# Kernel optimization log

Hardware: AMD Instinct MI355X
Metric: run time of the kernel (lower is better)

## Reference

```python
import math
import jax, jax.numpy as jnp
import numpy as np

B, T, E, H, D = 2, 2048, 1024, 16, 64


def setup_inputs() -> dict:
    key = jax.random.key(0)
    ks = jax.random.split(key, 6)
    x = jax.random.normal(ks[0], (B, T, E), dtype=jnp.float32)
    wr = jax.random.normal(ks[1], (H, E, T), dtype=jnp.float32) * math.sqrt(2.0 / E)
    wvr_w = jax.random.normal(ks[2], (H * D, E), dtype=jnp.float32) * (1.0 / math.sqrt(E))
    wj_w = jax.random.normal(ks[3], (E, E), dtype=jnp.float32) * (1.0 / math.sqrt(E))
    gate = jnp.zeros((H, 2), dtype=jnp.float32)
    wo_w = jax.random.normal(ks[4], (E, H * D), dtype=jnp.float32) * (1.0 / math.sqrt(H * D))
    return {"x": x, "wr": wr, "wvr_w": wvr_w, "wj_w": wj_w, "gate": gate, "wo_w": wo_w}


def reference(x, wr, wvr_w, wj_w, gate, wo_w):
    B_, T_, E_ = x.shape
    H_ = gate.shape[0]
    D_ = wvr_w.shape[0] // H_
    sc = 1.0 / math.sqrt(D_)
    mask = jnp.triu(jnp.ones((T_, T_), dtype=bool), k=1)  # True above diagonal

    # --- RRP branch: score-based causal attention with per-head learned key scores ---
    rv = (x @ wvr_w.T).reshape(B_, T_, H_, D_).transpose(0, 2, 1, 3)  # [B,H,T,D]
    ra = jnp.einsum('bte,het->bht', x, wr[:, :, :T_]) * sc            # [B,H,T]
    ra = jnp.where(mask, -jnp.inf, ra[:, :, None, :])                 # [B,H,T,T]
    rrp_out = jax.nn.softmax(ra, axis=-1) @ rv                        # [B,H,T,D]

    # --- Janus branch: outer-product shared attention over echoed features ---
    echo = x @ wj_w.T                                                 # [B,T,E]
    eb = echo @ wj_w                                                  # F.linear(echo, W.T)
    sc2 = (x * eb).sum(-1) / math.sqrt(E_)                            # [B,T]
    ja = jnp.where(mask, -jnp.inf, sc2[:, :, None] * sc2[:, None, :]) # [B,T,T]
    ja = jax.nn.softmax(ja, axis=-1)
    jan_out = jnp.einsum('bst,bthd->bhsd', ja, echo.reshape(B_, T_, H_, D_))  # [B,H,T,D]

    # --- Gated fusion per head ---
    g = jax.nn.softmax(gate, axis=-1)                                 # [H,2]
    out = (g[:, 0][None, :, None, None] * rrp_out
           + g[:, 1][None, :, None, None] * jan_out)                  # [B,H,T,D]
    out = out.transpose(0, 2, 1, 3).reshape(B_, T_, H_ * D_)
    return out @ wo_w.T
```

## Files before the change

### kernel.cpp

```cpp
#include <hip/hip_runtime.h>
#include <hip/hip_bf16.h>
#include <stdint.h>

#define B_    2
#define T_    2048
#define E_    1024
#define H_    16
#define D_    64
#define NTOK  (B_*T_)

typedef unsigned short u16;
typedef short s16x8 __attribute__((ext_vector_type(8)));
typedef float f32x4 __attribute__((ext_vector_type(4)));

__device__ __forceinline__ u16 f2bf(float f) {
  uint32_t u = __float_as_uint(f);
  u += 0x7FFFu + ((u >> 16) & 1u);
  return (u16)(u >> 16);
}
__device__ __forceinline__ float bf2f(u16 h) {
  return __uint_as_float(((uint32_t)h) << 16);
}
__device__ __forceinline__ void split2(float v, u16 &h, u16 &l) {
  h = f2bf(v);
  l = f2bf(v - bf2f(h));
}

__device__ __forceinline__ void gload_lds16(const void* g, void* l) {
  void* gnc = const_cast<void*>(g);
  __builtin_amdgcn_global_load_lds(
      (__attribute__((address_space(1))) uint32_t*)gnc,
      (__attribute__((address_space(3))) uint32_t*)l, 16, 0, 0);
}

#define MFMA_BF16(accv, av, bv) \
  asm("v_mfma_f32_16x16x32_bf16 %0, %1, %2, %0" : "+v"(accv) : "v"(av), "v"(bv))

__global__ __launch_bounds__(256) void k_split(const float* __restrict__ in,
                                               u16* __restrict__ hi,
                                               u16* __restrict__ lo, int n4) {
  int i = blockIdx.x * 256 + threadIdx.x;
  if (i >= n4) return;
  float4 v = ((const float4*)in)[i];
  u16 h0,h1,h2,h3,l0,l1,l2,l3;
  split2(v.x,h0,l0); split2(v.y,h1,l1); split2(v.z,h2,l2); split2(v.w,h3,l3);
  ushort4 hv; hv.x=h0; hv.y=h1; hv.z=h2; hv.w=h3;
  ushort4 lv; lv.x=l0; lv.y=l1; lv.z=l2; lv.w=l3;
  ((ushort4*)hi)[i] = hv;
  ((ushort4*)lo)[i] = lv;
}

template<int BN>
__global__ __launch_bounds__(256) void gemm_nt_split(
    const u16* __restrict__ Ahi, const u16* __restrict__ Alo,
    const u16* __restrict__ Bhi, const u16* __restrict__ Blo,
    float* __restrict__ C0, float* __restrict__ C1, int Nsplit, int ldC,
    int M, int N, int K,
    long long sA, long long sB, long long sC, int causal) {
  constexpr int NJ = BN / 32;
  const int bz = blockIdx.z;
  Ahi += (size_t)bz * sA; Alo += (size_t)bz * sA;
  Bhi += (size_t)bz * sB; Blo += (size_t)bz * sB;
  C0  += (size_t)bz * sC; C1  += (size_t)bz * sC;

  const int m0 = blockIdx.y * 128;
  const int n0 = blockIdx.x * BN;
  const int tid  = threadIdx.x;
  const int lane = tid & 63;
  const int w    = tid >> 6;
  const int wm = w >> 1, wn = w & 1;
  const int kmax = causal ? ((m0 + 128 < K) ? (m0 + 128) : K) : K;

  __shared__ u16 sAhi[128*32], sAlo[128*32], sBhi[BN*32], sBlo[BN*32];

  const int r0 = tid >> 2;
  const int c0 = (((tid & 3) ^ ((tid >> 3) & 3)) * 8);
  const int ldso = r0 * 32 + (tid & 3) * 8;
  const size_t arow  = (size_t)(m0 + r0) * K;
  const size_t arow2 = (size_t)(m0 + 64 + r0) * K;
  const size_t brow  = (size_t)(n0 + r0) * K;
  const size_t brow2 = (size_t)(n0 + 64 + r0) * K;

  f32x4 acc[4][NJ] = {};

  for (int k0 = 0; k0 < kmax; k0 += 32) {
    const int kc = k0 + c0;
    gload_lds16(Ahi + arow  + kc, &sAhi[ldso]);
    gload_lds16(Ahi + arow2 + kc, &sAhi[64*32 + ldso]);
    gload_lds16(Alo + arow  + kc, &sAlo[ldso]);
    gload_lds16(Alo + arow2 + kc, &sAlo[64*32 + ldso]);
    gload_lds16(Bhi + brow  + kc, &sBhi[ldso]);
    gload_lds16(Blo + brow  + kc, &sBlo[ldso]);
    if constexpr (BN == 128) {
      gload_lds16(Bhi + brow2 + kc, &sBhi[64*32 + ldso]);
      gload_lds16(Blo + brow2 + kc, &sBlo[64*32 + ldso]);
    }
    __syncthreads();

    const int la = lane & 15;
    const int kap = (((lane >> 4) ^ ((lane >> 1) & 3)) * 8);
    s16x8 ah[4], al[4], bh[NJ], bl[NJ];
    #pragma unroll
    for (int i = 0; i < 4; ++i) {
      const int ar = (wm*64 + i*16 + la) * 32 + kap;
      ah[i] = *(const s16x8*)&sAhi[ar];
      al[i] = *(const s16x8*)&sAlo[ar];
    }
    #pragma unroll
    for (int j = 0; j < NJ; ++j) {
      const int br = (wn*(BN/2) + j*16 + la) * 32 + kap;
      bh[j] = *(const s16x8*)&sBhi[br];
      bl[j] = *(const s16x8*)&sBlo[br];
    }
    #pragma unroll
    for (int i = 0; i < 4; ++i) {
      #pragma unroll
      for (int j = 0; j < NJ; ++j) {
        MFMA_BF16(acc[i][j], al[i], bh[j]);
        MFMA_BF16(acc[i][j], ah[i], bl[j]);
        MFMA_BF16(acc[i][j], ah[i], bh[j]);
      }
    }
    __syncthreads();
  }

  asm volatile("s_nop 7\n\ts_nop 7\n\ts_nop 7" ::);

  const int cr = (lane >> 4) * 4;
  const int cc = lane & 15;
  float* Cb = (n0 >= Nsplit) ? C1 : C0;
  const int nbase = (n0 >= Nsplit) ? n0 - Nsplit : n0;
  #pragma unroll
  for (int i = 0; i < 4; ++i) {
    #pragma unroll
    for (int j = 0; j < NJ; ++j) {
      const size_t row = (size_t)(m0 + wm*64 + i*16 + cr);
      const int col = nbase + wn*(BN/2) + j*16 + cc;
      float* cp = Cb + row * ldC + col;
      cp[0]               = acc[i][j][0];
      cp[(size_t)ldC]     = acc[i][j][1];
      cp[(size_t)2*ldC]   = acc[i][j][2];
      cp[(size_t)3*ldC]   = acc[i][j][3];
    }
  }
}

__global__ __launch_bounds__(256) void k_sc2(const float* __restrict__ echo,
                                             float* __restrict__ sc2) {
  int tok  = blockIdx.x * 4 + (threadIdx.x >> 6);
  int lane = threadIdx.x & 63;
  const float4* p = (const float4*)(echo + (size_t)tok * E_);
  float s = 0.f;
  #pragma unroll
  for (int j = 0; j < 4; ++j) {
    float4 v = p[lane + j*64];
    s += v.x*v.x + v.y*v.y + v.z*v.z + v.w*v.w;
  }
  #pragma unroll
  for (int off = 32; off; off >>= 1) s += __shfl_xor(s, off);
  if (lane == 0) sc2[tok] = s * (1.0f/32.0f);
}

__global__ __launch_bounds__(256) void k_tsplit(const float* __restrict__ echo,
                                                u16* __restrict__ Thi,
                                                u16* __restrict__ Tlo) {
  __shared__ float tile[32][33];
  int b = blockIdx.z;
  int t0 = blockIdx.x * 32, e0 = blockIdx.y * 32;
  int lx = threadIdx.x & 31, ly = threadIdx.x >> 5;
  #pragma unroll
  for (int i = 0; i < 32; i += 8)
    tile[ly + i][lx] = echo[((size_t)b*T_ + t0 + ly + i) * E_ + e0 + lx];
  __syncthreads();
  #pragma unroll
  for (int i = 0; i < 32; i += 8) {
    float v = tile[lx][ly + i];
    size_t o = ((size_t)b*E_ + e0 + ly + i) * T_ + t0 + lx;
    u16 h, l; split2(v, h, l);
    Thi[o] = h; Tlo[o] = l;
  }
}

__global__ __launch_bounds__(256) void k_ra(const float* __restrict__ x,
                                            const float* __restrict__ wr,
                                            float* __restrict__ ra) {
  __shared__ float xs[2][32][65];
  const int tid  = threadIdx.x;
  const int lane = tid & 63;
  const int t0 = blockIdx.x * 64;
  const int e0 = blockIdx.y * 32;
  const int h  = blockIdx.z * 4 + (tid >> 6);
  #pragma unroll
  for (int b = 0; b < 2; ++b)
    #pragma unroll
    for (int p = 0; p < 2; ++p) {
      const int ee = (tid & 3) * 4 + p * 16;
      const int tt = tid >> 2;
      float4 v = *(const float4*)&x[((size_t)b*T_ + t0 + tt) * E_ + e0 + ee];
      xs[b][ee+0][tt] = v.x; xs[b][ee+1][tt] = v.y;
      xs[b][ee+2][tt] = v.z; xs[b][ee+3][tt] = v.w;
    }
  __syncthreads();
  const float* wrp = wr + ((size_t)h * E_ + e0) * T_ + t0 + lane;
  float a0 = 0.f, a1 = 0.f;
  #pragma unroll 8
  for (int e = 0; e < 32; ++e) {
    float wv = wrp[(size_t)e * T_];
    a0 = fmaf(xs[0][e][lane], wv, a0);
    a1 = fmaf(xs[1][e][lane], wv, a1);
  }
  atomicAdd(&ra[(size_t)h * T_ + t0 + lane], a0);
  atomicAdd(&ra[(size_t)(H_ + h) * T_ + t0 + lane], a1);
}

__global__ __launch_bounds__(256) void k_gmax(const float* __restrict__ ra,
                                              float* __restrict__ gmaxb) {
  int bh = blockIdx.x;
  int tid = threadIdx.x;
  const float* rar = ra + (size_t)bh * T_;
  __shared__ float red[256];
  float mx = -1e30f;
  for (int t = tid; t < T_; t += 256) mx = fmaxf(mx, rar[t]);
  red[tid] = mx; __syncthreads();
  for (int s = 128; s > 0; s >>= 1) {
    if (tid < s) red[tid] = fmaxf(red[tid], red[tid + s]);
    __syncthreads();
  }
  if (tid == 0) gmaxb[bh] = red[0] * 0.125f;
}

__global__ __launch_bounds__(64) void k_csum(const float* __restrict__ ra,
    const float* __restrict__ rv, const float* __restrict__ gmaxb,
    float* __restrict__ csnum, float* __restrict__ csden) {
  int bh = blockIdx.x, c = blockIdx.y;
  int b = bh >> 4, h = bh & 15;
  int lane = threadIdx.x;
  float gm = gmaxb[bh];
  const float* rar = ra + (size_t)bh * T_;
  int t0 = c * 64;
  const float* rvp = rv + ((size_t)b * T_ + t0) * E_ + h * 64 + lane;
  float num = 0.f, den = 0.f;
  #pragma unroll 4
  for (int i = 0; i < 64; ++i) {
    float wt = __expf(fmaf(rar[t0 + i], 0.125f, -gm));
    num = fmaf(wt, rvp[(size_t)i * E_], num);
    den += wt;
  }
  csnum[((size_t)bh * 32 + c) * 64 + lane] = num;
  if (lane == 0) csden[bh * 32 + c] = den;
}

__global__ __launch_bounds__(64) void k_rrp2(const float* __restrict__ ra,
    const float* __restrict__ rv, const float* __restrict__ gmaxb,
    const float* __restrict__ csnum, const float* __restrict__ csden,
    float* __restrict__ rrp) {
  int bh = blockIdx.x, c = blockIdx.y;
  int b = bh >> 4, h = bh & 15;
  int lane = threadIdx.x;
  float gm = gmaxb[bh];
  const float* rar = ra + (size_t)bh * T_;
  float num = 0.f, den = 0.f;
  for (int cc = 0; cc < c; ++cc) {
    num += csnum[((size_t)bh * 32 + cc) * 64 + lane];
    den += csden[bh * 32 + cc];
  }
  int t0 = c * 64;
  const float* rvp = rv  + ((size_t)b * T_ + t0) * E_ + h * 64 + lane;
  float*       op  = rrp + ((size_t)b * T_ + t0) * E_ + h * 64 + lane;
  for (int i = 0; i < 64; ++i) {
    float wt = __expf(fmaf(rar[t0 + i], 0.125f, -gm));
    num = fmaf(wt, rvp[(size_t)i * E_], num);
    den += wt;
    op[(size_t)i * E_] = num / den;
  }
}

__global__ __launch_bounds__(256) void k_pmax(const float* __restrict__ sc2,
                                              float* __restrict__ pmax) {
  int b = blockIdx.x;
  __shared__ float u[T_];
  int tid = threadIdx.x;
  for (int i = tid; i < T_; i += 256) u[i] = sc2[b*T_ + i];
  __syncthreads();
  for (int off = 1; off < T_; off <<= 1) {
    float v[8];
    #pragma unroll
    for (int k = 0; k < 8; ++k) {
      int i = tid + k*256;
      v[k] = (i >= off) ? fmaxf(u[i], u[i-off]) : u[i];
    }
    __syncthreads();
    #pragma unroll
    for (int k = 0; k < 8; ++k) u[tid + k*256] = v[k];
    __syncthreads();
  }
  for (int i = tid; i < T_; i += 256) pmax[b*T_ + i] = u[i];
}

__global__ __launch_bounds__(256) void k_jden(const float* __restrict__ sc2,
    const float* __restrict__ pmax, float* __restrict__ jm,
    float* __restrict__ jden) {
  int b = blockIdx.y;
  int s = blockIdx.x * 4 + (threadIdx.x >> 6);
  int lane = threadIdx.x & 63;
  const float* u = sc2 + b*T_;
  float a = u[s];
  float m = a * pmax[b*T_ + s];
  float d = 0.f;
  for (int t = lane; t <= s; t += 64) d += __expf(fmaf(a, u[t], -m));
  #pragma unroll
  for (int off = 32; off; off >>= 1) d += __shfl_xor(d, off);
  if (lane == 0) { jm[b*T_+s] = m; jden[b*T_+s] = d; }
}

__global__ __launch_bounds__(256) void k_pgen(const float* __restrict__ sc2,
    const float* __restrict__ jm, const float* __restrict__ jden,
    u16* __restrict__ Phi, u16* __restrict__ Plo) {
  int b = blockIdx.z;
  size_t base = ((size_t)blockIdx.x * 256 + threadIdx.x) * 8;
  int s  = (int)(base >> 11);
  int t0 = (int)(base & 2047);
  const float* u = sc2 + b*T_;
  float a = u[s];
  float m = jm[b*T_+s];
  float invd = 1.0f / jden[b*T_+s];
  u16 hh[8], ll[8];
  #pragma unroll
  for (int k = 0; k < 8; ++k) {
    int tt = t0 + k;
    float p = (tt <= s) ? __expf(fmaf(a, u[tt], -m)) * invd : 0.0f;
    split2(p, hh[k], ll[k]);
  }
  size_t o = ((size_t)b*T_ + s) * T_ + t0;
  ushort4 h0; h0.x=hh[0]; h0.y=hh[1]; h0.z=hh[2]; h0.w=hh[3];
  ushort4 h1; h1.x=hh[4]; h1.y=hh[5]; h1.z=hh[6]; h1.w=hh[7];
  ushort4 l0; l0.x=ll[0]; l0.y=ll[1]; l0.z=ll[2]; l0.w=ll[3];
  ushort4 l1; l1.x=ll[4]; l1.y=ll[5]; l1.z=ll[6]; l1.w=ll[7];
  *(ushort4*)(Phi + o)     = h0; *(ushort4*)(Phi + o + 4) = h1;
  *(ushort4*)(Plo + o)     = l0; *(ushort4*)(Plo + o + 4) = l1;
}

__global__ __launch_bounds__(256) void k_fuse(const float* __restrict__ rrp,
    const float* __restrict__ jan, const float* __restrict__ gate,
    u16* __restrict__ Fhi, u16* __restrict__ Flo) {
  int i = blockIdx.x * 256 + threadIdx.x;
  int h = (i & 255) >> 4;
  float g0 = gate[h*2], g1 = gate[h*2+1];
  float mg = fmaxf(g0, g1);
  float e0 = __expf(g0 - mg), e1 = __expf(g1 - mg);
  float inv = 1.0f / (e0 + e1);
  float w0 = e0 * inv, w1 = e1 * inv;
  float4 r = ((const float4*)rrp)[i];
  float4 j = ((const float4*)jan)[i];
  u16 hh[4], ll[4];
  split2(w0*r.x + w1*j.x, hh[0], ll[0]);
  split2(w0*r.y + w1*j.y, hh[1], ll[1]);
  split2(w0*r.z + w1*j.z, hh[2], ll[2]);
  split2(w0*r.w + w1*j.w, hh[3], ll[3]);
  ushort4 hv; hv.x=hh[0]; hv.y=hh[1]; hv.z=hh[2]; hv.w=hh[3];
  ushort4 lv; lv.x=ll[0]; lv.y=ll[1]; lv.z=ll[2]; lv.w=ll[3];
  ((ushort4*)Fhi)[i] = hv;
  ((ushort4*)Flo)[i] = lv;
}

extern "C" void kernel_launch(void* const* d_in, const int* in_sizes, int n_in,
                              void* d_out, int out_size, void* d_ws, size_t ws_size,
                              hipStream_t stream) {
  const float* x    = (const float*)d_in[0];
  const float* wr   = (const float*)d_in[1];
  const float* wvr  = (const float*)d_in[2];
  const float* wj   = (const float*)d_in[3];
  const float* gate = (const float*)d_in[4];
  const float* wo   = (const float*)d_in[5];
  float* out = (float*)d_out;

  char* p = (char*)d_ws;
  auto alloc = [&](size_t bytes) {
    char* r = p;
    p += (bytes + 255) & ~(size_t)255;
    return r;
  };
  u16* x_hi   = (u16*)alloc((size_t)NTOK*E_*2);
  u16* x_lo   = (u16*)alloc((size_t)NTOK*E_*2);
  u16* wvr_hi = (u16*)alloc((size_t)E_*E_*2);
  u16* wj_hi  = (u16*)alloc((size_t)E_*E_*2);
  u16* wvr_lo = (u16*)alloc((size_t)E_*E_*2);
  u16* wj_lo  = (u16*)alloc((size_t)E_*E_*2);
  u16* wo_hi  = (u16*)alloc((size_t)E_*E_*2);
  u16* wo_lo  = (u16*)alloc((size_t)E_*E_*2);
  float* rv   = (float*)alloc((size_t)NTOK*E_*4);
  float* echo = (float*)alloc((size_t)NTOK*E_*4);
  u16* p_lo   = (u16*)alloc((size_t)B_*T_*T_*2);
  u16* eT_hi  = (u16*)alloc((size_t)B_*E_*T_*2);
  u16* eT_lo  = (u16*)alloc((size_t)B_*E_*T_*2);
  float* sc2  = (float*)alloc((size_t)NTOK*4);
  float* ra   = (float*)alloc((size_t)B_*H_*T_*4);
  float* gmaxb= (float*)alloc(32*4);
  float* csnum= (float*)alloc((size_t)32*32*64*4);
  float* csden= (float*)alloc((size_t)32*32*4);
  float* pmaxv= (float*)alloc((size_t)NTOK*4);
  float* jm   = (float*)alloc((size_t)NTOK*4);
  float* jden = (float*)alloc((size_t)NTOK*4);
  float* rrp  = (float*)alloc((size_t)NTOK*E_*4);
  u16* f_hi   = (u16*)alloc((size_t)NTOK*E_*2);
  u16* f_lo   = (u16*)alloc((size_t)NTOK*E_*2);
  u16* p_hi = (u16*)echo;
  float* jan = rv;

  int n4;
  n4 = NTOK*E_/4; k_split<<<dim3((n4+255)/256),256,0,stream>>>(x,   x_hi,   x_lo,   n4);
  n4 = E_*E_/4;   k_split<<<dim3((n4+255)/256),256,0,stream>>>(wvr, wvr_hi, wvr_lo, n4);
                  k_split<<<dim3((n4+255)/256),256,0,stream>>>(wj,  wj_hi,  wj_lo,  n4);
                  k_split<<<dim3((n4+255)/256),256,0,stream>>>(wo,  wo_hi,  wo_lo,  n4);

  gemm_nt_split<128><<<dim3(16,32,1),256,0,stream>>>(
      x_hi, x_lo, wvr_hi, wvr_lo, rv, echo, E_, E_,
      NTOK, 2*E_, E_, 0,0,0, 0);

  k_sc2<<<dim3(NTOK/4),256,0,stream>>>(echo, sc2);
  k_tsplit<<<dim3(T_/32, E_/32, B_),256,0,stream>>>(echo, eT_hi, eT_lo);

  hipMemsetAsync(ra, 0, (size_t)B_*H_*T_*4, stream);
  k_ra<<<dim3(T_/64, E_/32, H_/4),256,0,stream>>>(x, wr, ra);

  k_gmax<<<dim3(32),256,0,stream>>>(ra, gmaxb);
  k_csum<<<dim3(32,32),64,0,stream>>>(ra, rv, gmaxb, csnum, csden);
  k_rrp2<<<dim3(32,32),64,0,stream>>>(ra, rv, gmaxb, csnum, csden, rrp);

  k_pmax<<<dim3(B_),256,0,stream>>>(sc2, pmaxv);
  k_jden<<<dim3(T_/4, B_),256,0,stream>>>(sc2, pmaxv, jm, jden);
  k_pgen<<<dim3(T_*T_/2048, 1, B_),256,0,stream>>>(sc2, jm, jden, p_hi, p_lo);
  gemm_nt_split<64><<<dim3(16,16,2),256,0,stream>>>(
      p_hi, p_lo, eT_hi, eT_lo, jan, jan, 1<<30, E_,
      T_, E_, T_, (long long)T_*T_, (long long)E_*T_, (long long)T_*E_, 1);

  n4 = NTOK*E_/4;
  k_fuse<<<dim3(n4/256),256,0,stream>>>(rrp, jan, gate, f_hi, f_lo);
  gemm_nt_split<64><<<dim3(16,32,1),256,0,stream>>>(
      f_hi, f_lo, wo_hi, wo_lo, out, out, 1<<30, E_,
      NTOK, E_, E_, 0,0,0, 0);
}
```

Before: 458.5 us.

## Double-buffer split GEMM LDS tiles, widen RRP blocks, skip masked P tiles

The split-bf16 GEMM now uses two LDS buffers and prefetches the next K tile while computing the current one, dropping one barrier per iteration. k_csum and k_rrp2 pack four 64-lane chunks into each 256-thread block instead of one wave per block. k_pgen returns early for tiles above the causal diagonal (beyond the 128-aligned row block), which the causal GEMM never reads. Double buffering doubles LDS use, which may reduce occupancy.

```diff
diff --git a/kernel.cpp b/kernel.cpp
--- a/kernel.cpp
+++ b/kernel.cpp
@@ -71,57 +71,75 @@
   const int wm = w >> 1, wn = w & 1;
   const int kmax = causal ? ((m0 + 128 < K) ? (m0 + 128) : K) : K;
 
-  __shared__ u16 sAhi[128*32], sAlo[128*32], sBhi[BN*32], sBlo[BN*32];
+  __shared__ u16 sAhi[2][128*32], sAlo[2][128*32], sBhi[2][BN*32], sBlo[2][BN*32];
 
   const int r0 = tid >> 2;
   const int c0 = (((tid & 3) ^ ((tid >> 3) & 3)) * 8);
-  const int ldso = r0 * 32 + (tid & 3) * 8;
+  const int ldso = tid * 8;
   const size_t arow  = (size_t)(m0 + r0) * K;
   const size_t arow2 = (size_t)(m0 + 64 + r0) * K;
   const size_t brow  = (size_t)(n0 + r0) * K;
   const size_t brow2 = (size_t)(n0 + 64 + r0) * K;
 
   f32x4 acc[4][NJ] = {};
-
-  for (int k0 = 0; k0 < kmax; k0 += 32) {
-    const int kc = k0 + c0;
-    gload_lds16(Ahi + arow  + kc, &sAhi[ldso]);
-    gload_lds16(Ahi + arow2 + kc, &sAhi[64*32 + ldso]);
-    gload_lds16(Alo + arow  + kc, &sAlo[ldso]);
-    gload_lds16(Alo + arow2 + kc, &sAlo[64*32 + ldso]);
-    gload_lds16(Bhi + brow  + kc, &sBhi[ldso]);
-    gload_lds16(Blo + brow  + kc, &sBlo[ldso]);
+  const int nt = kmax >> 5;
+
+  {
+    const int kc = c0;
+    gload_lds16(Ahi + arow  + kc, &sAhi[0][ldso]);
+    gload_lds16(Ahi + arow2 + kc, &sAhi[0][64*32 + ldso]);
+    gload_lds16(Alo + arow  + kc, &sAlo[0][ldso]);
+    gload_lds16(Alo + arow2 + kc, &sAlo[0][64*32 + ldso]);
+    gload_lds16(Bhi + brow  + kc, &sBhi[0][ldso]);
+    gload_lds16(Blo + brow  + kc, &sBlo[0][ldso]);
     if constexpr (BN == 128) {
-      gload_lds16(Bhi + brow2 + kc, &sBhi[64*32 + ldso]);
-      gload_lds16(Blo + brow2 + kc, &sBlo[64*32 + ldso]);
-    }
+      gload_lds16(Bhi + brow2 + kc, &sBhi[0][64*32 + ldso]);
+      gload_lds16(Blo + brow2 + kc, &sBlo[0][64*32 + ldso]);
+    }
+  }
+
+  const int la = lane & 15;
+  const int kap = (((lane >> 4) ^ ((lane >> 1) & 3)) * 8);
+
+  for (int i = 0; i < nt; ++i) {
     __syncthreads();
-
-    const int la = lane & 15;
-    const int kap = (((lane >> 4) ^ ((lane >> 1) & 3)) * 8);
+    if (i + 1 < nt) {
+      const int nb = (i + 1) & 1;
+      const int kc = (i + 1) * 32 + c0;
+      gload_lds16(Ahi + arow  + kc, &sAhi[nb][ldso]);
+      gload_lds16(Ahi + arow2 + kc, &sAhi[nb][64*32 + ldso]);
+      gload_lds16(Alo + arow  + kc, &sAlo[nb][ldso]);
+      gload_lds16(Alo + arow2 + kc, &sAlo[nb][64*32 + ldso]);
+      gload_lds16(Bhi + brow  + kc, &sBhi[nb][ldso]);
+      gload_lds16(Blo + brow  + kc, &sBlo[nb][ldso]);
+      if constexpr (BN == 128) {
+        gload_lds16(Bhi + brow2 + kc, &sBhi[nb][64*32 + ldso]);
+        gload_lds16(Blo + brow2 + kc, &sBlo[nb][64*32 + ldso]);
+      }
+    }
+    const int cb = i & 1;
     s16x8 ah[4], al[4], bh[NJ], bl[NJ];
     #pragma unroll
-    for (int i = 0; i < 4; ++i) {
-      const int ar = (wm*64 + i*16 + la) * 32 + kap;
-      ah[i] = *(const s16x8*)&sAhi[ar];
-      al[i] = *(const s16x8*)&sAlo[ar];
+    for (int ii = 0; ii < 4; ++ii) {
+      const int ar = (wm*64 + ii*16 + la) * 32 + kap;
+      ah[ii] = *(const s16x8*)&sAhi[cb][ar];
+      al[ii] = *(const s16x8*)&sAlo[cb][ar];
     }
     #pragma unroll
     for (int j = 0; j < NJ; ++j) {
       const int br = (wn*(BN/2) + j*16 + la) * 32 + kap;
-      bh[j] = *(const s16x8*)&sBhi[br];
-      bl[j] = *(const s16x8*)&sBlo[br];
-    }
-    #pragma unroll
-    for (int i = 0; i < 4; ++i) {
+      bh[j] = *(const s16x8*)&sBhi[cb][br];
+      bl[j] = *(const s16x8*)&sBlo[cb][br];
+    }
+    #pragma unroll
+    for (int ii = 0; ii < 4; ++ii) {
       #pragma unroll
       for (int j = 0; j < NJ; ++j) {
-        MFMA_BF16(acc[i][j], al[i], bh[j]);
-        MFMA_BF16(acc[i][j], ah[i], bl[j]);
-        MFMA_BF16(acc[i][j], ah[i], bh[j]);
+        MFMA_BF16(acc[ii][j], al[ii], bh[j]);
+        MFMA_BF16(acc[ii][j], ah[ii], bl[j]);
+        MFMA_BF16(acc[ii][j], ah[ii], bh[j]);
       }
     }
-    __syncthreads();
   }
 
   asm volatile("s_nop 7\n\ts_nop 7\n\ts_nop 7" ::);
@@ -229,12 +247,13 @@
   if (tid == 0) gmaxb[bh] = red[0] * 0.125f;
 }
 
-__global__ __launch_bounds__(64) void k_csum(const float* __restrict__ ra,
+__global__ __launch_bounds__(256) void k_csum(const float* __restrict__ ra,
     const float* __restrict__ rv, const float* __restrict__ gmaxb,
     float* __restrict__ csnum, float* __restrict__ csden) {
-  int bh = blockIdx.x, c = blockIdx.y;
+  int bh = blockIdx.x;
+  int c  = blockIdx.y * 4 + (threadIdx.x >> 6);
   int b = bh >> 4, h = bh & 15;
-  int lane = threadIdx.x;
+  int lane = threadIdx.x & 63;
   float gm = gmaxb[bh];
   const float* rar = ra + (size_t)bh * T_;
   int t0 = c * 64;
@@ -250,13 +269,14 @@
   if (lane == 0) csden[bh * 32 + c] = den;
 }
 
-__global__ __launch_bounds__(64) void k_rrp2(const float* __restrict__ ra,
+__global__ __launch_bounds__(256) void k_rrp2(const float* __restrict__ ra,
     const float* __restrict__ rv, const float* __restrict__ gmaxb,
     const float* __restrict__ csnum, const float* __restrict__ csden,
     float* __restrict__ rrp) {
-  int bh = blockIdx.x, c = blockIdx.y;
+  int bh = blockIdx.x;
+  int c  = blockIdx.y * 4 + (threadIdx.x >> 6);
   int b = bh >> 4, h = bh & 15;
-  int lane = threadIdx.x;
+  int lane = threadIdx.x & 63;
   float gm = gmaxb[bh];
   const float* rar = ra + (size_t)bh * T_;
   float num = 0.f, den = 0.f;
@@ -320,6 +340,7 @@
   size_t base = ((size_t)blockIdx.x * 256 + threadIdx.x) * 8;
   int s  = (int)(base >> 11);
   int t0 = (int)(base & 2047);
+  if (t0 > (s | 127)) return;
   const float* u = sc2 + b*T_;
   float a = u[s];
   float m = jm[b*T_+s];
@@ -424,8 +445,8 @@
   k_ra<<<dim3(T_/64, E_/32, H_/4),256,0,stream>>>(x, wr, ra);
 
   k_gmax<<<dim3(32),256,0,stream>>>(ra, gmaxb);
-  k_csum<<<dim3(32,32),64,0,stream>>>(ra, rv, gmaxb, csnum, csden);
-  k_rrp2<<<dim3(32,32),64,0,stream>>>(ra, rv, gmaxb, csnum, csden, rrp);
+  k_csum<<<dim3(32,8),256,0,stream>>>(ra, rv, gmaxb, csnum, csden);
+  k_rrp2<<<dim3(32,8),256,0,stream>>>(ra, rv, gmaxb, csnum, csden, rrp);
 
   k_pmax<<<dim3(B_),256,0,stream>>>(sc2, pmaxv);
   k_jden<<<dim3(T_/4, B_),256,0,stream>>>(sc2, pmaxv, jm, jden);
```

Result: no change. 465.4 us (+1.5%).
